# Optimization experiments

Measured on AMD Instinct MI355X. Metric: run time of the kernel, lower is better.

Reference implementation:

```python
import jax, jax.numpy as jnp
import numpy as np

TAG = 64
START = 0
END = 1
NEG = -10000.0


def setup_inputs() -> dict:
    key = jax.random.key(0)
    kf, kw, kl = jax.random.split(key, 3)
    B, T, K = 1024, 512, TAG
    feats = jax.random.normal(kf, (B, T, K), dtype=jnp.float32)
    w = jax.random.uniform(kw, (K, K), minval=-1.0 / K, maxval=1.0 / K, dtype=jnp.float32)
    # default adjacency: forbid transitions into start (row START) and out of end (col END)
    adj = jnp.zeros((K, K), jnp.float32).at[START, :].set(1.0).at[:, END].set(1.0)
    weights = w + NEG * adj
    lens = jax.random.randint(kl, (B,), 1, T + 1)  # 1..T inclusive
    return {"feats": feats, "weights": weights, "lens": lens}


def reference(feats, weights, lens):
    # feats: [B, T, K], weights: [K, K] with weights[next, prev], lens: [B]
    B, T, K = feats.shape
    init = jnp.full((B, K), NEG, feats.dtype).at[:, START].set(0.0)
    mask_tb = (jnp.arange(T)[None, :] < lens[:, None]).T  # [T, B]
    ident = jnp.arange(K, dtype=jnp.int32)

    def step(fv, inp):
        feat, m = inp  # feat: [B, K], m: [B]
        scores = fv[:, None, :] + weights[None, :, :]  # [B, next, prev]
        new_fv = jnp.max(scores, axis=-1) + feat       # emission added after max
        bptr = jnp.argmax(scores, axis=-1).astype(jnp.int32)
        fv2 = jnp.where(m[:, None], new_fv, fv)
        bptr2 = jnp.where(m[:, None], bptr, ident[None, :])  # identity keeps backtrace valid past len
        return fv2, bptr2

    fv, bptrs = jax.lax.scan(step, init, (jnp.swapaxes(feats, 0, 1), mask_tb))
    terminal = fv + weights[END][None, :]              # transition to end tag
    best_last = jnp.argmax(terminal, axis=-1)
    path_score = jnp.take_along_axis(terminal, best_last[:, None], axis=1)[:, 0]

    def back(tag, bp):  # tag: [B], bp: [B, K]
        prev = jnp.take_along_axis(bp, tag[:, None], axis=1)[:, 0]
        return prev, tag  # emit tag chosen at this timestep

    _, path = jax.lax.scan(back, best_last.astype(jnp.int32), bptrs, reverse=True)
    best_paths = jnp.swapaxes(path, 0, 1)  # [B, T]; positions >= lens[b] are padding
    return path_score, best_paths
```

## Files before the change

### kernel.cpp

```cpp
#include <hip/hip_runtime.h>

#define TAGS 64
#define MAXT 512
#define NEG  -10000.0f
#define CH   8

__global__ __launch_bounds__(192) void crf_viterbi(
    const float* __restrict__ feats,
    const float* __restrict__ weights,
    const int*   __restrict__ lens,
    float*       __restrict__ out,
    int B, int T)
{
    const int b    = blockIdx.x;
    const int tid  = threadIdx.x;
    const int wv   = tid >> 6;
    const int lane = tid & 63;
    const int len  = lens[b];

    __shared__ float fbuf[2][CH * TAGS];
    __shared__ float pub[3][CH][2][TAGS];
    __shared__ unsigned char  bptr[MAXT * TAGS];
    __shared__ unsigned short path[MAXT];

#define F3(a, b, c) fmaxf(fmaxf((a), (b)), (c))
#define M3(a, b, c) min(min((a), (b)), (c))

    float4 w4[16];
    #pragma unroll
    for (int i = 0; i < 16; ++i)
        w4[i] = *reinterpret_cast<const float4*>(weights + lane * TAGS + i * 4);
    const float wEnd = weights[1 * TAGS + lane];

    const float* fb  = feats + (size_t)b * T * TAGS;
    const int    lim = len * TAGS - 4;
    const int    nch = (len + CH - 1) / CH;

    float nf = NEG;
    float4 n0 = {0,0,0,0}, n1 = {0,0,0,0};
    int cb = 0;

    if (wv == 0) {
        pub[2][CH - 1][0][lane] = (lane == 0) ? 0.0f : NEG;
        int o0 = 4 * lane;        if (o0 > lim) o0 = lim;
        int o1 = 256 + 4 * lane;  if (o1 > lim) o1 = lim;
        *reinterpret_cast<float4*>(&fbuf[0][4 * lane])       = *reinterpret_cast<const float4*>(fb + o0);
        *reinterpret_cast<float4*>(&fbuf[0][256 + 4 * lane]) = *reinterpret_cast<const float4*>(fb + o1);
        int p0 = CH * TAGS + 4 * lane;        if (p0 > lim) p0 = lim;
        int p1 = CH * TAGS + 256 + 4 * lane;  if (p1 > lim) p1 = lim;
        n0 = *reinterpret_cast<const float4*>(fb + p0);
        n1 = *reinterpret_cast<const float4*>(fb + p1);
    }
    __syncthreads();

    int m0 = 0;
    for (int c = 0; c <= nch; ++c) {
        const int m1 = (m0 == 0) ? 2 : m0 - 1;
        const int m2 = (m0 == 2) ? 0 : m0 + 1;

        if (wv == 0) {
            if (c < nch) {
                const int n = min(CH, len - c * CH);
                float*       pw  = &pub[m0][0][0][0];
                const float* pr0 = &pub[m1][CH - 1][0][0];
                #pragma unroll
                for (int i = 0; i < CH; ++i) {
                    if (i < n) {
                        const float feat = fbuf[cb][i * TAGS + lane];
                        const float* fvp = (i == 0) ? pr0 : (pw + (i - 1) * 2 * TAGS);
                        float4 fq[16];
                        #pragma unroll
                        for (int g = 0; g < 16; ++g)
                            fq[g] = *reinterpret_cast<const float4*>(fvp + 4 * g);
                        float4 c4[16];
                        #pragma unroll
                        for (int g = 0; g < 16; ++g) {
                            c4[g].x = fq[g].x + w4[g].x;
                            c4[g].y = fq[g].y + w4[g].y;
                            c4[g].z = fq[g].z + w4[g].z;
                            c4[g].w = fq[g].w + w4[g].w;
                        }
                        const float* cc = reinterpret_cast<const float*>(c4);
                        float v1[22];
                        #pragma unroll
                        for (int k = 0; k < 21; ++k) v1[k] = F3(cc[3*k], cc[3*k+1], cc[3*k+2]);
                        v1[21] = cc[63];
                        float v2[8];
                        #pragma unroll
                        for (int k = 0; k < 7; ++k) v2[k] = F3(v1[3*k], v1[3*k+1], v1[3*k+2]);
                        v2[7] = v1[21];
                        const float v30 = F3(v2[0], v2[1], v2[2]);
                        const float v31 = F3(v2[3], v2[4], v2[5]);
                        const float v32 = fmaxf(v2[6], v2[7]);
                        const float m   = F3(v30, v31, v32);

                        nf = m + feat;
                        pw[i * 2 * TAGS + lane]        = nf;
                        pw[i * 2 * TAGS + TAGS + lane] = m;
                    }
                }
                *reinterpret_cast<float4*>(&fbuf[cb ^ 1][4 * lane])       = n0;
                *reinterpret_cast<float4*>(&fbuf[cb ^ 1][256 + 4 * lane]) = n1;
                int q0 = (c + 2) * CH * TAGS + 4 * lane;        if (q0 > lim) q0 = lim;
                int q1 = (c + 2) * CH * TAGS + 256 + 4 * lane;  if (q1 > lim) q1 = lim;
                n0 = *reinterpret_cast<const float4*>(fb + q0);
                n1 = *reinterpret_cast<const float4*>(fb + q1);
                cb ^= 1;
            }
        } else if (c > 0) {
            const int ck = c - 1;
            const int n  = min(CH, len - ck * CH);
            const float* prd = &pub[m1][0][0][0];
            const float* pr0 = &pub[m2][CH - 1][0][0];
            for (int i = wv - 1; i < n; i += 2) {
                const float* fvp = (i == 0) ? pr0 : (prd + (i - 1) * 2 * TAGS);
                const float  mm  = prd[i * 2 * TAGS + TAGS + lane];
                unsigned q[16];
                #pragma unroll
                for (int g = 0; g < 16; ++g) {
                    const float4 fq = *reinterpret_cast<const float4*>(fvp + 4 * g);
                    const float cx = fq.x + w4[g].x;
                    const float cy = fq.y + w4[g].y;
                    const float cz = fq.z + w4[g].z;
                    const float cw = fq.w + w4[g].w;
                    const unsigned k0 = (__float_as_uint(mm - cx) & 0xFFFFFFC0u) | (unsigned)(4*g+0);
                    const unsigned k1 = (__float_as_uint(mm - cy) & 0xFFFFFFC0u) | (unsigned)(4*g+1);
                    const unsigned k2 = (__float_as_uint(mm - cz) & 0xFFFFFFC0u) | (unsigned)(4*g+2);
                    const unsigned k3 = (__float_as_uint(mm - cw) & 0xFFFFFFC0u) | (unsigned)(4*g+3);
                    q[g] = min(M3(k0, k1, k2), k3);
                }
                const unsigned t0 = M3(q[0],  q[1],  q[2]);
                const unsigned t1 = M3(q[3],  q[4],  q[5]);
                const unsigned t2 = M3(q[6],  q[7],  q[8]);
                const unsigned t3 = M3(q[9],  q[10], q[11]);
                const unsigned t4 = M3(q[12], q[13], q[14]);
                const unsigned s0 = M3(t0, t1, t2);
                const unsigned s1 = M3(t3, t4, q[15]);
                const unsigned idx = min(s0, s1);
                bptr[(ck * CH + i) * TAGS + lane] = (unsigned char)idx;
            }
        }
        __syncthreads();
        m0 = m2;
    }

    if (wv != 0) return;

    float tv = nf + wEnd;
    int   ti = lane;
    #pragma unroll
    for (int off = 32; off >= 1; off >>= 1) {
        const float ov = __shfl_xor(tv, off);
        const int   oi = __shfl_xor(ti, off);
        if (ov > tv || (ov == tv && oi < ti)) { tv = ov; ti = oi; }
    }
    if (lane == 0) out[b] = tv;
    const int bestlast = ti;

    for (int t = lane; t < T; t += 64)
        if (t >= len - 1) path[t] = (unsigned short)bestlast;
    __builtin_amdgcn_wave_barrier();

    if (lane == 0) {
        int tag = bestlast;
        for (int t = len - 1; t >= 1; --t) {
            tag = bptr[t * TAGS + tag];
            path[t - 1] = (unsigned short)tag;
        }
    }
    __builtin_amdgcn_wave_barrier();

    float* pout = out + B + (size_t)b * T;
    for (int t = lane; t < T; t += 64)
        pout[t] = (float)path[t];
}

extern "C" void kernel_launch(void* const* d_in, const int* in_sizes, int n_in,
                              void* d_out, int out_size, void* d_ws, size_t ws_size,
                              hipStream_t stream) {
    const float* feats   = (const float*)d_in[0];
    const float* weights = (const float*)d_in[1];
    const int*   lens    = (const int*)d_in[2];
    float*       out     = (float*)d_out;

    const int B = in_sizes[2];
    const int T = in_sizes[0] / (B * TAGS);

    crf_viterbi<<<dim3(B), dim3(192), 0, stream>>>(feats, weights, lens, out, B, T);
}
```

Baseline: 500.4 us.

## Shorten the serial wave's critical path by moving max recomputation to helper waves

The serial Viterbi wave no longer writes the per-step max to shared memory. It keeps emission features in registers, prefetching the next chunk straight from global memory instead of staging it through an LDS double buffer. The two backpointer waves now recompute the max themselves from the shared forward vectors. A small three-slot seed buffer carries the last forward vector across chunks, and launch bounds now request one block per CU. The goal is to remove LDS traffic from the latency-bound recurrence, at the cost of more arithmetic and register pressure in the helper waves.

```diff
diff --git a/kernel.cpp b/kernel.cpp
--- a/kernel.cpp
+++ b/kernel.cpp
@@ -5,7 +5,7 @@
 #define NEG  -10000.0f
 #define CH   8
 
-__global__ __launch_bounds__(192) void crf_viterbi(
+__global__ __launch_bounds__(192, 1) void crf_viterbi(
     const float* __restrict__ feats,
     const float* __restrict__ weights,
     const int*   __restrict__ lens,
@@ -18,8 +18,8 @@
     const int lane = tid & 63;
     const int len  = lens[b];
 
-    __shared__ float fbuf[2][CH * TAGS];
-    __shared__ float pub[3][CH][2][TAGS];
+    __shared__ float pub[2][CH][TAGS];
+    __shared__ float seed[3][TAGS];
     __shared__ unsigned char  bptr[MAXT * TAGS];
     __shared__ unsigned short path[MAXT];
 
@@ -33,41 +33,39 @@
     const float wEnd = weights[1 * TAGS + lane];
 
     const float* fb  = feats + (size_t)b * T * TAGS;
-    const int    lim = len * TAGS - 4;
+    const int    cap = len * TAGS;
     const int    nch = (len + CH - 1) / CH;
 
     float nf = NEG;
-    float4 n0 = {0,0,0,0}, n1 = {0,0,0,0};
-    int cb = 0;
+    float fcur[CH], fnx[CH];
 
     if (wv == 0) {
-        pub[2][CH - 1][0][lane] = (lane == 0) ? 0.0f : NEG;
-        int o0 = 4 * lane;        if (o0 > lim) o0 = lim;
-        int o1 = 256 + 4 * lane;  if (o1 > lim) o1 = lim;
-        *reinterpret_cast<float4*>(&fbuf[0][4 * lane])       = *reinterpret_cast<const float4*>(fb + o0);
-        *reinterpret_cast<float4*>(&fbuf[0][256 + 4 * lane]) = *reinterpret_cast<const float4*>(fb + o1);
-        int p0 = CH * TAGS + 4 * lane;        if (p0 > lim) p0 = lim;
-        int p1 = CH * TAGS + 256 + 4 * lane;  if (p1 > lim) p1 = lim;
-        n0 = *reinterpret_cast<const float4*>(fb + p0);
-        n1 = *reinterpret_cast<const float4*>(fb + p1);
-    }
-    __syncthreads();
-
-    int m0 = 0;
+        const float init = (lane == 0) ? 0.0f : NEG;
+        pub[1][CH - 1][lane] = init;
+        seed[2][lane]        = init;
+        #pragma unroll
+        for (int i = 0; i < CH; ++i) {
+            int o = i * TAGS + lane; if (o >= cap) o = lane;
+            fcur[i] = fb[o];
+        }
+        #pragma unroll
+        for (int i = 0; i < CH; ++i) {
+            int o = (CH + i) * TAGS + lane; if (o >= cap) o = lane;
+            fnx[i] = fb[o];
+        }
+    }
+
+    int m3 = 0;
     for (int c = 0; c <= nch; ++c) {
-        const int m1 = (m0 == 0) ? 2 : m0 - 1;
-        const int m2 = (m0 == 2) ? 0 : m0 + 1;
-
         if (wv == 0) {
             if (c < nch) {
-                const int n = min(CH, len - c * CH);
-                float*       pw  = &pub[m0][0][0][0];
-                const float* pr0 = &pub[m1][CH - 1][0][0];
+                const int    n     = min(CH, len - c * CH);
+                float*       cur   = &pub[c & 1][0][0];
+                const float* prev0 = &pub[(c + 1) & 1][CH - 1][0];
                 #pragma unroll
                 for (int i = 0; i < CH; ++i) {
                     if (i < n) {
-                        const float feat = fbuf[cb][i * TAGS + lane];
-                        const float* fvp = (i == 0) ? pr0 : (pw + (i - 1) * 2 * TAGS);
+                        const float* fvp = (i == 0) ? prev0 : (cur + (i - 1) * TAGS);
                         float4 fq[16];
                         #pragma unroll
                         for (int g = 0; g < 16; ++g)
@@ -94,39 +92,54 @@
                         const float v32 = fmaxf(v2[6], v2[7]);
                         const float m   = F3(v30, v31, v32);
 
-                        nf = m + feat;
-                        pw[i * 2 * TAGS + lane]        = nf;
-                        pw[i * 2 * TAGS + TAGS + lane] = m;
+                        nf = m + fcur[i];
+                        cur[i * TAGS + lane] = nf;
                     }
                 }
-                *reinterpret_cast<float4*>(&fbuf[cb ^ 1][4 * lane])       = n0;
-                *reinterpret_cast<float4*>(&fbuf[cb ^ 1][256 + 4 * lane]) = n1;
-                int q0 = (c + 2) * CH * TAGS + 4 * lane;        if (q0 > lim) q0 = lim;
-                int q1 = (c + 2) * CH * TAGS + 256 + 4 * lane;  if (q1 > lim) q1 = lim;
-                n0 = *reinterpret_cast<const float4*>(fb + q0);
-                n1 = *reinterpret_cast<const float4*>(fb + q1);
-                cb ^= 1;
+                seed[m3][lane] = nf;
+                #pragma unroll
+                for (int i = 0; i < CH; ++i) fcur[i] = fnx[i];
+                #pragma unroll
+                for (int i = 0; i < CH; ++i) {
+                    int o = (c + 2) * CH * TAGS + i * TAGS + lane;
+                    if (o >= cap) o = lane;
+                    fnx[i] = fb[o];
+                }
             }
         } else if (c > 0) {
-            const int ck = c - 1;
-            const int n  = min(CH, len - ck * CH);
-            const float* prd = &pub[m1][0][0][0];
-            const float* pr0 = &pub[m2][CH - 1][0][0];
+            const int    ck    = c - 1;
+            const int    n     = min(CH, len - ck * CH);
+            const float* base  = &pub[ck & 1][0][0];
+            const float* prev0 = &seed[(m3 + 1) % 3][0];
             for (int i = wv - 1; i < n; i += 2) {
-                const float* fvp = (i == 0) ? pr0 : (prd + (i - 1) * 2 * TAGS);
-                const float  mm  = prd[i * 2 * TAGS + TAGS + lane];
-                unsigned q[16];
+                const float* fvp = (i == 0) ? prev0 : (base + (i - 1) * TAGS);
+                float cv[64];
                 #pragma unroll
                 for (int g = 0; g < 16; ++g) {
                     const float4 fq = *reinterpret_cast<const float4*>(fvp + 4 * g);
-                    const float cx = fq.x + w4[g].x;
-                    const float cy = fq.y + w4[g].y;
-                    const float cz = fq.z + w4[g].z;
-                    const float cw = fq.w + w4[g].w;
-                    const unsigned k0 = (__float_as_uint(mm - cx) & 0xFFFFFFC0u) | (unsigned)(4*g+0);
-                    const unsigned k1 = (__float_as_uint(mm - cy) & 0xFFFFFFC0u) | (unsigned)(4*g+1);
-                    const unsigned k2 = (__float_as_uint(mm - cz) & 0xFFFFFFC0u) | (unsigned)(4*g+2);
-                    const unsigned k3 = (__float_as_uint(mm - cw) & 0xFFFFFFC0u) | (unsigned)(4*g+3);
+                    cv[4*g+0] = fq.x + w4[g].x;
+                    cv[4*g+1] = fq.y + w4[g].y;
+                    cv[4*g+2] = fq.z + w4[g].z;
+                    cv[4*g+3] = fq.w + w4[g].w;
+                }
+                float v1[22];
+                #pragma unroll
+                for (int k = 0; k < 21; ++k) v1[k] = F3(cv[3*k], cv[3*k+1], cv[3*k+2]);
+                v1[21] = cv[63];
+                float v2[8];
+                #pragma unroll
+                for (int k = 0; k < 7; ++k) v2[k] = F3(v1[3*k], v1[3*k+1], v1[3*k+2]);
+                v2[7] = v1[21];
+                const float mm = F3(F3(v2[0], v2[1], v2[2]),
+                                    F3(v2[3], v2[4], v2[5]),
+                                    fmaxf(v2[6], v2[7]));
+                unsigned q[16];
+                #pragma unroll
+                for (int g = 0; g < 16; ++g) {
+                    const unsigned k0 = (__float_as_uint(mm - cv[4*g+0]) & 0xFFFFFFC0u) | (unsigned)(4*g+0);
+                    const unsigned k1 = (__float_as_uint(mm - cv[4*g+1]) & 0xFFFFFFC0u) | (unsigned)(4*g+1);
+                    const unsigned k2 = (__float_as_uint(mm - cv[4*g+2]) & 0xFFFFFFC0u) | (unsigned)(4*g+2);
+                    const unsigned k3 = (__float_as_uint(mm - cv[4*g+3]) & 0xFFFFFFC0u) | (unsigned)(4*g+3);
                     q[g] = min(M3(k0, k1, k2), k3);
                 }
                 const unsigned t0 = M3(q[0],  q[1],  q[2]);
@@ -134,14 +147,12 @@
                 const unsigned t2 = M3(q[6],  q[7],  q[8]);
                 const unsigned t3 = M3(q[9],  q[10], q[11]);
                 const unsigned t4 = M3(q[12], q[13], q[14]);
-                const unsigned s0 = M3(t0, t1, t2);
-                const unsigned s1 = M3(t3, t4, q[15]);
-                const unsigned idx = min(s0, s1);
+                const unsigned idx = min(M3(t0, t1, t2), M3(t3, t4, q[15]));
                 bptr[(ck * CH + i) * TAGS + lane] = (unsigned char)idx;
             }
         }
         __syncthreads();
-        m0 = m2;
+        m3 = (m3 == 2) ? 0 : m3 + 1;
     }
 
     if (wv != 0) return;
```

After: 542.7 us. 1.08x slower.
